# Kernel tuning notes

Measured on AMD Instinct MI355X. Metric: run time of the kernel, lower is better.

## Reference

```python
import jax, jax.numpy as jnp
import numpy as np

H = W = 256
C = 128
SCALE = 512 ** (-0.5)  # literal from the source, not 1/sqrt(C)


def _pool_mat(size, out):
    # adaptive_avg_pool1d matrix: row i averages input[start_i:end_i]
    i = np.arange(out)
    s = (i * size) // out
    e = ((i + 1) * size + out - 1) // out  # ceil
    P = np.zeros((out, size), np.float32)
    for k in range(out):
        P[k, s[k]:e[k]] = 1.0 / (e[k] - s[k])
    return jnp.asarray(P)


def adaptive_avg_pool2d(x, out):
    # x: [B, C, H, W] -> [B, C, out, out] via separable pooling matrices
    Ph = _pool_mat(x.shape[2], out)
    Pw = _pool_mat(x.shape[3], out)
    y = jnp.einsum('oh,bchw->bcow', Ph, x)
    return jnp.einsum('pw,bcow->bcop', Pw, y)


def setup_inputs() -> dict:
    key = jax.random.key(0)
    k1, k2 = jax.random.split(key)
    x5 = jax.random.normal(k1, (4, C, H, W), dtype=jnp.float32)
    W_out = jax.random.normal(k2, (C, C), dtype=jnp.float32) * 0.02
    b_out = jnp.zeros((C,), dtype=jnp.float32)
    return {"x5": x5, "W_out": W_out, "b_out": b_out}


def reference(x5, W_out, b_out):
    B = x5.shape[0]
    # Query: [B, N, C], N = H*W
    Query = x5.reshape(B, C, H * W).transpose(0, 2, 1)
    # multi-scale pooled keys
    p16 = adaptive_avg_pool2d(x5, 16)
    p12 = adaptive_avg_pool2d(x5, 12)
    p9 = adaptive_avg_pool2d(x5, 9)
    p7 = adaptive_avg_pool2d(x5, 7)
    p6 = adaptive_avg_pool2d(x5, 6)
    p3 = adaptive_avg_pool2d(x5, 3)
    p1 = adaptive_avg_pool2d(x5, 1)
    # Key: concat flattened pools in source order [3, 1, 9, 7, 16] -> [B, C, 396]
    Key = jnp.concatenate(
        [p.reshape(B, C, -1) for p in (p3, p1, p9, p7, p16)], axis=-1)
    Value = Key.transpose(0, 2, 1)  # [B, 396, C]
    # attention: [B, N, 396]
    attn = jax.nn.softmax(SCALE * jnp.einsum('bnc,bck->bnk', Query, Key), axis=-1)
    agg = jnp.einsum('bnk,bkc->bnc', attn, Value)  # [B, N, C]
    agg = agg.transpose(0, 2, 1).reshape(B, C, H, W)
    # 1x1 conv
    out = jnp.einsum('oc,bchw->bohw', W_out, agg) + b_out[None, :, None, None]
    return (out + x5, p12, p6)
```

## Files before the change

### kernel.cpp

```cpp
#include <hip/hip_runtime.h>
#include <hip/hip_bf16.h>

typedef short bf16x8 __attribute__((ext_vector_type(8)));
typedef float f32x4  __attribute__((ext_vector_type(4)));
typedef unsigned short u16;

#define B_N 4
#define C_N 128
#define HW_ 256
#define NPIX 65536
#define NK 396
#define NKP 400
#define OUT_MAIN ((size_t)B_N * C_N * NPIX)
#define P12_OFF OUT_MAIN
#define P6_OFF  (P12_OFF + (size_t)B_N * C_N * 144)

#define BUFSZ  32768
#define VT_OFF 16384
#define P_OFF  65536
#define LDS_BYTES 73728

static __device__ __forceinline__ u16 f2bf(float x) {
  __hip_bfloat16 h = __float2bfloat16(x);
  return *(u16*)&h;
}
static __device__ __forceinline__ unsigned pack2(float lo, float hi) {
  return ((unsigned)f2bf(hi) << 16) | f2bf(lo);
}
static __device__ __forceinline__ void gl_lds16(const void* g, void* l) {
  __builtin_amdgcn_global_load_lds(
      (const __attribute__((address_space(1))) unsigned*)g,
      (__attribute__((address_space(3))) unsigned*)l, 16, 0, 0);
}
#define MFMA32 __builtin_amdgcn_mfma_f32_16x16x32_bf16
#define LGKM0 do { asm volatile("s_waitcnt lgkmcnt(0)" ::: "memory"); \
                   __builtin_amdgcn_sched_barrier(0); } while (0)

__global__ __launch_bounds__(1024) void pool_kernel(
    const float* __restrict__ x5, const float* __restrict__ W_out,
    u16* __restrict__ wsK, u16* __restrict__ wsKT, u16* __restrict__ wsW,
    float* __restrict__ out)
{
  __shared__ float yh[54][257];
  const int tid = threadIdx.x;
  const int bc = blockIdx.x;
  const int b  = bc >> 7;
  const int c  = bc & 127;
  const float2* plane2 = (const float2*)(x5 + (size_t)bc * NPIX);
  const int w2 = tid & 127;
  const int q  = tid >> 7;
  const int h0 = q * 32;

  if (bc < 16) {
    const int idx = bc * 1024 + tid;
    wsW[idx] = f2bf(W_out[idx]);
  }

  for (int i = tid; i < 54 * 257; i += 1024) ((float*)yh)[i] = 0.f;
  __syncthreads();

  const int os_[7] = {16,12,9,7,6,3,1};
  const int ro_[7] = {0,16,28,37,44,50,53};
  float ax[7], ay[7], a2x[7], a2y[7], inv_[7];
  int r_[7], e_[7], s2_[7];
  #pragma unroll
  for (int s = 0; s < 7; ++s) {
    const int o = os_[s];
    const int r = (h0 * o) >> 8;
    const int sr = (r * 256) / o;
    r_[s]  = r;
    e_[s]  = ((r + 1) * 256 + o - 1) / o;
    s2_[s] = ((r + 1) * 256) / o;
    inv_[s] = 1.0f / (float)(e_[s] - sr);
    ax[s] = 0.f; ay[s] = 0.f; a2x[s] = 0.f; a2y[s] = 0.f;
  }

  #pragma unroll
  for (int g = 0; g < 4; ++g) {
    float2 vv[8];
    #pragma unroll
    for (int k = 0; k < 8; ++k) vv[k] = plane2[(h0 + g*8 + k) * 128 + w2];
    #pragma unroll
    for (int k = 0; k < 8; ++k) {
      const int h = h0 + g*8 + k;
      const float2 v = vv[k];
      #pragma unroll
      for (int s = 0; s < 7; ++s) {
        const int o = os_[s];
        ax[s] += v.x; ay[s] += v.y;
        if (h >= s2_[s]) { a2x[s] += v.x; a2y[s] += v.y; }
        if (h + 1 == e_[s]) {
          atomicAdd(&yh[ro_[s] + r_[s]][2*w2],     ax[s] * inv_[s]);
          atomicAdd(&yh[ro_[s] + r_[s]][2*w2 + 1], ay[s] * inv_[s]);
          r_[s]++;
          const int sr = s2_[s];
          e_[s]  = ((r_[s] + 1) * 256 + o - 1) / o;
          s2_[s] = ((r_[s] + 1) * 256) / o;
          inv_[s] = 1.0f / (float)(e_[s] - sr);
          ax[s] = a2x[s]; ay[s] = a2y[s];
          a2x[s] = 0.f; a2y[s] = 0.f;
        }
      }
    }
  }
  #pragma unroll
  for (int s = 0; s < 7; ++s) {
    const int o = os_[s];
    if (r_[s] < o) {
      atomicAdd(&yh[ro_[s] + r_[s]][2*w2],     ax[s] * inv_[s]);
      atomicAdd(&yh[ro_[s] + r_[s]][2*w2 + 1], ay[s] * inv_[s]);
      if (r_[s] + 1 < o && s2_[s] < h0 + 32) {
        const int sr2 = s2_[s];
        const int e2  = ((r_[s] + 2) * 256 + o - 1) / o;
        const float inv2 = 1.0f / (float)(e2 - sr2);
        atomicAdd(&yh[ro_[s] + r_[s] + 1][2*w2],     a2x[s] * inv2);
        atomicAdd(&yh[ro_[s] + r_[s] + 1][2*w2 + 1], a2y[s] * inv2);
      }
    }
  }
  __syncthreads();

  if (tid < NKP - NK) {
    wsK [((size_t)b * NKP + NK + tid) * C_N + c] = 0;
    wsKT[(size_t)bc * NKP + NK + tid] = 0;
  }

  for (int r = tid; r < 576; r += 1024) {
    int rr = r;
    int o, ro, kbase, dst;
    if      (rr < 256) { o = 16; ro = 0;  kbase = 140; dst = 0; }
    else if (rr < 400) { o = 12; ro = 16; kbase = 0;   dst = 1; rr -= 256; }
    else if (rr < 481) { o = 9;  ro = 28; kbase = 10;  dst = 0; rr -= 400; }
    else if (rr < 530) { o = 7;  ro = 37; kbase = 91;  dst = 0; rr -= 481; }
    else if (rr < 566) { o = 6;  ro = 44; kbase = 0;   dst = 2; rr -= 530; }
    else if (rr < 575) { o = 3;  ro = 50; kbase = 0;   dst = 0; rr -= 566; }
    else               { o = 1;  ro = 53; kbase = 9;   dst = 0; rr = 0;   }
    const int i = rr / o;
    const int j = rr - i * o;
    const int s = (j * HW_) / o;
    const int e = ((j + 1) * HW_ + o - 1) / o;
    float sum = 0.f;
    const float* row = yh[ro + i];
    for (int wq = s; wq < e; ++wq) sum += row[wq];
    const float v = sum * (1.0f / (float)(e - s));
    if (dst == 1) {
      out[P12_OFF + (size_t)bc * 144 + rr] = v;
    } else if (dst == 2) {
      out[P6_OFF + (size_t)bc * 36 + rr] = v;
    } else {
      const int key = kbase + rr;
      const u16 bv = f2bf(v);
      wsK [((size_t)b * NKP + key) * C_N + c] = bv;
      wsKT[(size_t)bc * NKP + key]            = bv;
    }
  }
}

template<int CB, int BUF>
static __device__ __forceinline__ void stage64(
    char* smem, const char* wsKb, const char* wsKTb, int wv, int lane)
{
  char* buf = smem + BUF * BUFSZ;
  #pragma unroll
  for (int j = 0; j < 4; ++j) {
    const int krow = CB + j*16 + wv*4 + (lane >> 4);
    gl_lds16(wsKb + (size_t)krow * 256 + (((lane & 15) ^ (krow & 15)) << 4),
             buf + j*4096 + wv*1024);
    const int vrow = j*32 + wv*8 + (lane >> 3);
    gl_lds16(wsKTb + (size_t)vrow * (NKP*2) + CB*2 + (((lane & 7) ^ (vrow & 7)) << 4),
             buf + VT_OFF + j*4096 + wv*1024);
  }
}

static __device__ __forceinline__ void stage_tail(
    char* buf, const char* wsKb, const char* wsKTb, int wv, int lane)
{
  {
    const int row = wv*4 + (lane >> 4);
    gl_lds16(wsKb + (size_t)(384 + row) * 256 + (((lane & 15) ^ (row & 15)) << 4),
             buf + wv * 1024);
  }
  #pragma unroll
  for (int j = 0; j < 2; ++j) {
    const int row = j*64 + wv*16 + (lane >> 2);
    gl_lds16(wsKTb + (size_t)row * (NKP*2) + 768 + ((lane & 3) << 4),
             buf + VT_OFF + j*4096 + wv*1024);
  }
}

static __device__ __forceinline__ void stage_W(
    char* smem, const u16* wsW, int wv, int lane)
{
  #pragma unroll
  for (int j = 0; j < 8; ++j) {
    const int row = j*16 + wv*4 + (lane >> 4);
    gl_lds16((const char*)wsW + (size_t)row * 256 + (((lane & 15) ^ (row & 15)) << 4),
             smem + BUFSZ + j*4096 + wv*1024);
  }
}

template<int BUF, int TAIL>
static __device__ __forceinline__ void compute64(
    char* smem, char* pbase, const bf16x8 (&qf)[2][4],
    f32x4 (&agg)[8][2], float (&d)[2], int l15, int l4)
{
  const char* buf = smem + BUF * BUFSZ;
  constexpr int NT   = TAIL ? 1 : 4;
  constexpr int SUBS = TAIL ? 1 : 2;

  f32x4 sA[NT][2];
  #pragma unroll
  for (int nt = 0; nt < NT; ++nt) {
    sA[nt][0] = (f32x4){0.f,0.f,0.f,0.f};
    sA[nt][1] = (f32x4){0.f,0.f,0.f,0.f};
  }
  #pragma unroll
  for (int nt = 0; nt < NT; ++nt) {
    bf16x8 kf[4];
    #pragma unroll
    for (int kc = 0; kc < 4; ++kc)
      kf[kc] = *(const bf16x8*)(buf + (nt*16 + l15) * 256 +
                                ((kc*64 + l4*16) ^ (l15 << 4)));
    #pragma unroll
    for (int kc = 0; kc < 4; ++kc) {
      sA[nt][0] = MFMA32(kf[kc], qf[0][kc], sA[nt][0], 0, 0, 0);
      sA[nt][1] = MFMA32(kf[kc], qf[1][kc], sA[nt][1], 0, 0, 0);
    }
  }

  #pragma unroll
  for (int sub = 0; sub < SUBS; ++sub) {
    if (sub) LGKM0;
    #pragma unroll
    for (int pt = 0; pt < 2; ++pt) {
      const int prow = pt*16 + l15;
      const int sz2  = (prow & 3) << 4;
      #pragma unroll
      for (int u = 0; u < (TAIL ? 1 : 2); ++u) {
        const int nt = sub*2 + u;
        float p[4];
        #pragma unroll
        for (int qi = 0; qi < 4; ++qi) {
          float e = exp2f(sA[nt][pt][qi]);
          if (TAIL && (l4*4 + qi >= 12)) e = 0.f;
          p[qi] = e;
        }
        d[pt] += (p[0] + p[1]) + (p[2] + p[3]);
        uint2 pk;
        pk.x = pack2(p[0], p[1]);
        pk.y = pack2(p[2], p[3]);
        *(uint2*)(pbase + prow*64 + ((u*32 + l4*8) ^ sz2)) = pk;
      }
      if (TAIL) {
        uint2 z; z.x = 0u; z.y = 0u;
        *(uint2*)(pbase + prow*64 + ((32 + l4*8) ^ sz2)) = z;
      }
    }
    LGKM0;

    bf16x8 pf[2];
    #pragma unroll
    for (int pt = 0; pt < 2; ++pt) {
      const int prow = pt*16 + l15;
      pf[pt] = *(const bf16x8*)(pbase + prow*64 + ((l4*16) ^ ((prow & 3) << 4)));
    }
    #pragma unroll
    for (int ct = 0; ct < 8; ++ct) {
      const int vrow = ct*16 + l15;
      bf16x8 vf;
      if (TAIL)
        vf = *(const bf16x8*)(buf + VT_OFF + vrow*64 + l4*16);
      else
        vf = *(const bf16x8*)(buf + VT_OFF + vrow*128 +
                              ((sub*64 + l4*16) ^ ((vrow & 7) << 4)));
      agg[ct][0] = MFMA32(vf, pf[0], agg[ct][0], 0, 0, 0);
      agg[ct][1] = MFMA32(vf, pf[1], agg[ct][1], 0, 0, 0);
    }
  }
}

__global__ __launch_bounds__(256, 2) void attn_kernel(
    const float* __restrict__ x5, const u16* __restrict__ wsK,
    const u16* __restrict__ wsKT, const u16* __restrict__ wsW,
    const float* __restrict__ b_out, float* __restrict__ out)
{
  extern __shared__ char smem[];
  const int tid  = threadIdx.x;
  const int wgid = (blockIdx.x & 7) * 256 + (blockIdx.x >> 3);
  const int b    = wgid >> 9;
  const int pix0 = (wgid & 511) << 7;
  const int lane = tid & 63, wv = tid >> 6;
  const int l15  = lane & 15, l4 = lane >> 4;
  const float SCL2 = 0.044194173824159216f * 1.4426950408889634f;
  char* pbase = smem + P_OFF + wv * 2048;

  const char* wsKb  = (const char*)wsK  + (size_t)b * NKP * C_N * 2;
  const char* wsKTb = (const char*)wsKT + (size_t)b * C_N * NKP * 2;

  {
    const float* r0p = x5 + (((size_t)(b * C_N + 2*lane)) << 16) + pix0 + wv * 32;
    const float* r1p = r0p + NPIX;
    float4 v0[8], v1[8];
    #pragma unroll
    for (int j = 0; j < 8; ++j) {
      v0[j] = *(const float4*)(r0p + j*4);
      v1[j] = *(const float4*)(r1p + j*4);
    }
    #pragma unroll
    for (int i = 0; i < 32; ++i) {
      const int pix = wv * 32 + i;
      const unsigned pk = pack2(((const float*)&v0[i>>2])[i&3] * SCL2,
                                ((const float*)&v1[i>>2])[i&3] * SCL2);
      *(unsigned*)(smem + pix * 256 + ((lane*4) ^ ((pix & 15) << 4))) = pk;
    }
  }
  __syncthreads();

  bf16x8 qf[2][4];
  #pragma unroll
  for (int pt = 0; pt < 2; ++pt)
    #pragma unroll
    for (int kc = 0; kc < 4; ++kc)
      qf[pt][kc] = *(const bf16x8*)(smem + (wv*32 + pt*16 + l15) * 256 +
                                    ((kc*64 + l4*16) ^ (l15 << 4)));
  __syncthreads();

  f32x4 agg[8][2];
  #pragma unroll
  for (int ct = 0; ct < 8; ++ct) {
    agg[ct][0] = (f32x4){0.f,0.f,0.f,0.f};
    agg[ct][1] = (f32x4){0.f,0.f,0.f,0.f};
  }
  float d[2] = {0.f, 0.f};

  stage64<0, 0>(smem, wsKb, wsKTb, wv, lane);
  asm volatile("s_waitcnt vmcnt(0)" ::: "memory");
  __syncthreads();

  stage64<64, 1>(smem, wsKb, wsKTb, wv, lane);
  compute64<0, 0>(smem, pbase, qf, agg, d, l15, l4);
  asm volatile("s_waitcnt vmcnt(0)" ::: "memory");
  __syncthreads();

  stage64<128, 0>(smem, wsKb, wsKTb, wv, lane);
  compute64<1, 0>(smem, pbase, qf, agg, d, l15, l4);
  asm volatile("s_waitcnt vmcnt(0)" ::: "memory");
  __syncthreads();

  stage64<192, 1>(smem, wsKb, wsKTb, wv, lane);
  compute64<0, 0>(smem, pbase, qf, agg, d, l15, l4);
  asm volatile("s_waitcnt vmcnt(0)" ::: "memory");
  __syncthreads();

  stage64<256, 0>(smem, wsKb, wsKTb, wv, lane);
  compute64<1, 0>(smem, pbase, qf, agg, d, l15, l4);
  asm volatile("s_waitcnt vmcnt(0)" ::: "memory");
  __syncthreads();

  stage64<320, 1>(smem, wsKb, wsKTb, wv, lane);
  compute64<0, 0>(smem, pbase, qf, agg, d, l15, l4);
  asm volatile("s_waitcnt vmcnt(0)" ::: "memory");
  __syncthreads();

  stage_tail(smem, wsKb, wsKTb, wv, lane);
  compute64<1, 0>(smem, pbase, qf, agg, d, l15, l4);
  asm volatile("s_waitcnt vmcnt(0)" ::: "memory");
  __syncthreads();

  {
    f32x4 z = (f32x4){0.f,0.f,0.f,0.f};
    *(f32x4*)(smem + VT_OFF + (tid >> 1) * 64 + 32 + ((tid & 1) << 4)) = z;
  }
  stage_W(smem, wsW, wv, lane);
  asm volatile("s_waitcnt vmcnt(0)" ::: "memory");
  __syncthreads();

  compute64<0, 1>(smem, pbase, qf, agg, d, l15, l4);

  float inv[2];
  #pragma unroll
  for (int pt = 0; pt < 2; ++pt) {
    float s = d[pt];
    s += __shfl_xor(s, 16);
    s += __shfl_xor(s, 32);
    inv[pt] = 1.0f / s;
  }

  f32x4 cacc[8][2];
  #pragma unroll
  for (int ot = 0; ot < 8; ++ot) {
    cacc[ot][0] = (f32x4){0.f,0.f,0.f,0.f};
    cacc[ot][1] = (f32x4){0.f,0.f,0.f,0.f};
  }
  #pragma unroll
  for (int qh = 0; qh < 4; ++qh) {
    LGKM0;
    #pragma unroll
    for (int pt = 0; pt < 2; ++pt) {
      const int prow = pt*16 + l15;
      const int sz2  = (prow & 3) << 4;
      #pragma unroll
      for (int u = 0; u < 2; ++u) {
        const f32x4 a = agg[qh*2 + u][pt];
        uint2 pk;
        pk.x = pack2(a[0] * inv[pt], a[1] * inv[pt]);
        pk.y = pack2(a[2] * inv[pt], a[3] * inv[pt]);
        *(uint2*)(pbase + prow*64 + ((u*32 + l4*8) ^ sz2)) = pk;
      }
    }
    LGKM0;
    bf16x8 agf[2];
    #pragma unroll
    for (int pt = 0; pt < 2; ++pt) {
      const int prow = pt*16 + l15;
      agf[pt] = *(const bf16x8*)(pbase + prow*64 + ((l4*16) ^ ((prow & 3) << 4)));
    }
    #pragma unroll
    for (int ot = 0; ot < 8; ++ot) {
      const bf16x8 wa = *(const bf16x8*)(smem + BUFSZ + (ot*16 + l15) * 256 +
                                         ((qh*64 + l4*16) ^ (l15 << 4)));
      cacc[ot][0] = MFMA32(wa, agf[0], cacc[ot][0], 0, 0, 0);
      cacc[ot][1] = MFMA32(wa, agf[1], cacc[ot][1], 0, 0, 0);
    }
  }

  #pragma unroll
  for (int ot = 0; ot < 8; ++ot) {
    const float4 bq = *(const float4*)(b_out + ot*16 + l4*4);
    #pragma unroll
    for (int pt = 0; pt < 2; ++pt) {
      #pragma unroll
      for (int qi = 0; qi < 4; ++qi) {
        const int o = ot*16 + l4*4 + qi;
        const size_t idx = (((size_t)(b * C_N + o)) << 16) + pix0 + wv*32 + pt*16 + l15;
        out[idx] = cacc[ot][pt][qi] + ((const float*)&bq)[qi] + x5[idx];
      }
    }
  }
}

extern "C" void kernel_launch(void* const* d_in, const int* in_sizes, int n_in,
                              void* d_out, int out_size, void* d_ws, size_t ws_size,
                              hipStream_t stream) {
  const float* x5    = (const float*)d_in[0];
  const float* W_out = (const float*)d_in[1];
  const float* b_out = (const float*)d_in[2];
  float* out = (float*)d_out;
  u16* wsKT = (u16*)d_ws;
  u16* wsK  = (u16*)((char*)d_ws + (size_t)B_N * C_N * NKP * 2);
  u16* wsW  = (u16*)((char*)d_ws + (size_t)2 * B_N * C_N * NKP * 2);

  pool_kernel<<<512, 1024, 0, stream>>>(x5, W_out, wsK, wsKT, wsW, out);

  hipFuncSetAttribute((const void*)attn_kernel,
                      hipFuncAttributeMaxDynamicSharedMemorySize, LDS_BYTES);
  attn_kernel<<<B_N * 512, 256, LDS_BYTES, stream>>>(x5, wsK, wsKT, wsW, b_out, out);
}
```

Before: 205.5 us.

## Keep one K/V stage load in flight and parallelize pooled-cell reductions

The attention loop now issues the next stage's global-to-LDS loads before waiting, and uses partial vmcnt waits (vmcnt(8)/vmcnt(3)) plus raw barriers, so one buffer's loads overlap the previous buffer's compute instead of draining all loads every step. Separately, the pool kernel's final cell reduction assigns 16 lanes per output cell with shuffle reductions instead of one thread serially summing up to 256 elements. The risk is correctness of the vmcnt counts if stage64 or stage_tail issue a different number of loads than assumed, and the extra barrier after compute adds synchronization.

```diff
diff --git a/kernel.cpp b/kernel.cpp
--- a/kernel.cpp
+++ b/kernel.cpp
@@ -34,6 +34,12 @@
 }
 #define MFMA32 __builtin_amdgcn_mfma_f32_16x16x32_bf16
 #define LGKM0 do { asm volatile("s_waitcnt lgkmcnt(0)" ::: "memory"); \
+                   __builtin_amdgcn_sched_barrier(0); } while (0)
+#define BAR() do { __builtin_amdgcn_s_barrier(); \
+                   __builtin_amdgcn_sched_barrier(0); } while (0)
+#define VM8() do { asm volatile("s_waitcnt vmcnt(8)" ::: "memory"); \
+                   __builtin_amdgcn_sched_barrier(0); } while (0)
+#define VM3() do { asm volatile("s_waitcnt vmcnt(3)" ::: "memory"); \
                    __builtin_amdgcn_sched_barrier(0); } while (0)
 
 __global__ __launch_bounds__(1024) void pool_kernel(
@@ -125,7 +131,11 @@
     wsKT[(size_t)bc * NKP + NK + tid] = 0;
   }
 
-  for (int r = tid; r < 576; r += 1024) {
+  const int grp = tid >> 4;
+  const int gl  = tid & 15;
+  #pragma unroll
+  for (int it = 0; it < 9; ++it) {
+    const int r = grp + it * 64;
     int rr = r;
     int o, ro, kbase, dst;
     if      (rr < 256) { o = 16; ro = 0;  kbase = 140; dst = 0; }
@@ -139,19 +149,25 @@
     const int j = rr - i * o;
     const int s = (j * HW_) / o;
     const int e = ((j + 1) * HW_ + o - 1) / o;
-    float sum = 0.f;
+    float partial = 0.f;
     const float* row = yh[ro + i];
-    for (int wq = s; wq < e; ++wq) sum += row[wq];
-    const float v = sum * (1.0f / (float)(e - s));
-    if (dst == 1) {
-      out[P12_OFF + (size_t)bc * 144 + rr] = v;
-    } else if (dst == 2) {
-      out[P6_OFF + (size_t)bc * 36 + rr] = v;
-    } else {
-      const int key = kbase + rr;
-      const u16 bv = f2bf(v);
-      wsK [((size_t)b * NKP + key) * C_N + c] = bv;
-      wsKT[(size_t)bc * NKP + key]            = bv;
+    for (int wq = s + gl; wq < e; wq += 16) partial += row[wq];
+    partial += __shfl_xor(partial, 1);
+    partial += __shfl_xor(partial, 2);
+    partial += __shfl_xor(partial, 4);
+    partial += __shfl_xor(partial, 8);
+    if (gl == 0) {
+      const float v = partial * (1.0f / (float)(e - s));
+      if (dst == 1) {
+        out[P12_OFF + (size_t)bc * 144 + rr] = v;
+      } else if (dst == 2) {
+        out[P6_OFF + (size_t)bc * 36 + rr] = v;
+      } else {
+        const int key = kbase + rr;
+        const u16 bv = f2bf(v);
+        wsK [((size_t)b * NKP + key) * C_N + c] = bv;
+        wsKT[(size_t)bc * NKP + key]            = bv;
+      }
     }
   }
 }
@@ -334,38 +350,35 @@
   float d[2] = {0.f, 0.f};
 
   stage64<0, 0>(smem, wsKb, wsKTb, wv, lane);
-  asm volatile("s_waitcnt vmcnt(0)" ::: "memory");
-  __syncthreads();
-
   stage64<64, 1>(smem, wsKb, wsKTb, wv, lane);
+  VM8(); BAR();
   compute64<0, 0>(smem, pbase, qf, agg, d, l15, l4);
-  asm volatile("s_waitcnt vmcnt(0)" ::: "memory");
-  __syncthreads();
+  BAR();
 
   stage64<128, 0>(smem, wsKb, wsKTb, wv, lane);
+  VM8(); BAR();
   compute64<1, 0>(smem, pbase, qf, agg, d, l15, l4);
-  asm volatile("s_waitcnt vmcnt(0)" ::: "memory");
-  __syncthreads();
+  BAR();
 
   stage64<192, 1>(smem, wsKb, wsKTb, wv, lane);
+  VM8(); BAR();
   compute64<0, 0>(smem, pbase, qf, agg, d, l15, l4);
-  asm volatile("s_waitcnt vmcnt(0)" ::: "memory");
-  __syncthreads();
+  BAR();
 
   stage64<256, 0>(smem, wsKb, wsKTb, wv, lane);
+  VM8(); BAR();
   compute64<1, 0>(smem, pbase, qf, agg, d, l15, l4);
-  asm volatile("s_waitcnt vmcnt(0)" ::: "memory");
-  __syncthreads();
+  BAR();
 
   stage64<320, 1>(smem, wsKb, wsKTb, wv, lane);
+  VM8(); BAR();
   compute64<0, 0>(smem, pbase, qf, agg, d, l15, l4);
-  asm volatile("s_waitcnt vmcnt(0)" ::: "memory");
-  __syncthreads();
+  BAR();
 
   stage_tail(smem, wsKb, wsKTb, wv, lane);
+  VM3(); BAR();
   compute64<1, 0>(smem, pbase, qf, agg, d, l15, l4);
-  asm volatile("s_waitcnt vmcnt(0)" ::: "memory");
-  __syncthreads();
+  BAR();
 
   {
     f32x4 z = (f32x4){0.f,0.f,0.f,0.f};
```

New measurement: 205.0 us. About the same (-0.2%).
